# Kernel tuning notes

Hardware: AMD Instinct MI355X
Metric: run time of the kernel (lower is better)

Reference implementation:

```python
import jax, jax.numpy as jnp
import numpy as np

B, T = 256, 1024
IN_DIM, OUT_DIM = 32, 32
STATE_DIM, DIM_NL = 128, 128
EPS = 1e-3            # pos_def_tol
ALPHA = 1.0           # contraction_rate_lb
STD = 0.5             # initialization_std


def setup_inputs() -> dict:
    key = jax.random.key(0)
    ks = jax.random.split(key, 9)
    f = lambda k, sh: jax.random.normal(k, sh, dtype=jnp.float32)
    n, q = STATE_DIM, DIM_NL
    return {
        "x0_sys": f(ks[0], (B, 1, OUT_DIM)),
        "u_in": f(ks[1], (B, T, IN_DIM)),
        "X": f(ks[2], (2 * n + q, 2 * n + q)) * STD,
        "Y": f(ks[3], (n, n)) * STD,
        "B2": f(ks[4], (n, IN_DIM)) * STD,
        "C2": f(ks[5], (OUT_DIM, n)) * STD,
        "D21": f(ks[6], (OUT_DIM, q)) * STD,
        "D22": f(ks[7], (OUT_DIM, IN_DIM)) * STD,
        "D12": f(ks[8], (q, IN_DIM)) * STD,
    }


def _derived(X, Y):
    # Contraction-preserving reparametrization ("_update_model_param").
    n, q = STATE_DIM, DIM_NL
    H = X.T @ X + EPS * jnp.eye(2 * n + q, dtype=X.dtype)
    H11 = H[:n, :n]
    H21 = H[n:n + q, :n]
    H22 = H[n:n + q, n:n + q]
    H31 = H[n + q:, :n]
    H32 = H[n + q:, n:n + q]
    H33 = H[n + q:, n + q:]          # P
    F_ = H31
    B1 = H32
    E = 0.5 * (H11 + ALPHA * H33 + Y - Y.T)
    E_inv = jnp.linalg.inv(E)
    Lam = 0.5 * jnp.diag(H22)
    D11 = -jnp.tril(H22, -1)          # strictly lower triangular
    C1 = -H21
    return F_, B1, E_inv, Lam, D11, C1


def reference(x0_sys, u_in, X, Y, B2, C2, D21, D22, D12):
    F_, B1, E_inv, Lam, D11, C1 = _derived(X, Y)
    q = DIM_NL

    # reset(): x0 = min-norm lstsq solution of C2 x0 = y0_sys  (lstsq == pinv here)
    y0_sys = x0_sys[:, 0, :]                       # (B, out)
    x0 = (jnp.linalg.pinv(C2) @ y0_sys.T).T        # (B, n)
    y0 = x0 @ C2.T                                 # (B, out)

    idx = jnp.arange(q)

    def step(x, u):
        # one REN forward step; x:(B,n), u:(B,in)
        a = x @ C1.T + u @ D12.T                   # (B, q), i-independent part of v

        def inner(w, inp):
            i, d_row, lam, a_i = inp               # a_i:(B,)
            v = a_i + w @ d_row                    # strictly-lower-tri recurrence on w
            return w.at[:, i].set(jnp.tanh(v / lam)), None

        w0 = jnp.zeros((x.shape[0], q), x.dtype)
        w, _ = jax.lax.scan(inner, w0, (idx, D11, Lam, a.T))
        x_new = (x @ F_.T + w @ B1.T + u @ B2.T) @ E_inv.T
        y = x_new @ C2.T + w @ D21.T + u @ D22.T
        return x_new, y

    _, ys = jax.lax.scan(step, x0, jnp.swapaxes(u_in, 0, 1))   # (T, B, out)
    # run() emits y0 then outputs after u[0..T-2] (last step's y is dropped)
    y_traj = jnp.concatenate([y0[None], ys[:-1]], axis=0)      # (T, B, out)
    return jnp.swapaxes(y_traj, 0, 1)                          # (B, T, out)
```

## Files before the change

### kernel.cpp

```cpp
#include <hip/hip_runtime.h>
#include <hip/hip_bf16.h>

#define DEV static __device__ __forceinline__

constexpr int Tn = 1024;
constexpr float LOG2E = 1.4426950408889634f;

constexpr int OFF_H     = 0;
constexpr int OFF_E     = 147456;
constexpr int OFF_EINV  = 163840;
constexpr int OFF_M     = 180224;
constexpr int OFF_MINV  = 181248;
constexpr int OFF_GL2   = 182272;
constexpr int OFF_FH    = 182400;
constexpr int OFF_B1H   = 198784;
constexpr int OFF_B2H   = 215168;
constexpr int OFF_W0    = 219264;
constexpr int OFF_WC    = 223360;
constexpr int OFF_CF    = 227456;
constexpr int OFF_CB    = 243840;
constexpr int OFF_CB2   = 260224;
constexpr int OFF_PF    = 264320;
constexpr int OFF_PB    = 280704;
constexpr int OFF_PCF   = 297088;
constexpr int OFF_PCB   = 313472;
constexpr int OFF_SAB   = 329856;
constexpr int OFF_SB2   = 338048;
constexpr int OFF_BUQ   = 342144;
constexpr int OFF_D12Q  = 346240;
constexpr int OFF_SCB2  = 350336;
constexpr int OFF_WCS   = 354432;
constexpr int OFF_C2Y   = 358528;
constexpr int OFF_D21Y  = 362624;
constexpr int OFF_D22Y  = 366720;
constexpr int OFF_AUG   = 367744;
constexpr int OFF_AUG2  = 400512;
constexpr int OFF_X0    = 402560;
constexpr int OFF_A0    = 435328;
constexpr int WS_FLOATS = 468096;

__device__ __align__(16) float g_ws[WS_FLOATS];
__device__ int g_isf32;
__device__ float4 g_Q [256 * 1024 * 64];
__device__ float2 g_Xs[256 * 1024 * 64];
__device__ float2 g_Ws[256 * 1024 * 64];

DEV float ld(const void* p, int i, int f) {
  return f ? ((const float*)p)[i]
           : __bfloat162float(((const __hip_bfloat16*)p)[i]);
}
DEV float rdlane(float v, int l) {
  return __int_as_float(__builtin_amdgcn_readlane(__float_as_int(v), l));
}

__global__ void k_detect(const void* __restrict__ X) {
  if (threadIdx.x == 0) {
    const __hip_bfloat16* p = (const __hip_bfloat16*)X;
    int bad = 0;
    for (int i = 0; i < 512; ++i) {
      float v = __bfloat162float(p[i]);
      if (!(v > -1e6f && v < 1e6f)) bad++;
    }
    g_isf32 = (bad > 0) ? 1 : 0;
  }
}

__global__ void k_H(const void* __restrict__ X) {
  const int f = g_isf32;
  float* ws = g_ws;
  int id = blockIdx.x * 256 + threadIdx.x;
  int r = id / 384, c = id % 384;
  float acc = 0.f;
  for (int k = 0; k < 384; ++k)
    acc = fmaf(ld(X, k * 384 + r, f), ld(X, k * 384 + c, f), acc);
  if (r == c) acc += 0.001f;
  ws[OFF_H + id] = acc;
}

__global__ void k_derived(const void* __restrict__ Y, const void* __restrict__ C2) {
  const int f = g_isf32;
  float* ws = g_ws;
  const float* H = ws + OFF_H;
  int id = blockIdx.x * 256 + threadIdx.x;
  if (id < 16384) {
    int i = id >> 7, j = id & 127;
    ws[OFF_E + id] = 0.5f * (H[i * 384 + j] + H[(256 + i) * 384 + 256 + j]
                             + ld(Y, i * 128 + j, f) - ld(Y, j * 128 + i, f));
  } else if (id < 16512) {
    int i = id - 16384;
    ws[OFF_GL2 + i] = LOG2E * 4.f / H[(128 + i) * 384 + 128 + i];
  } else if (id < 17536) {
    int t = id - 16512; int a = t >> 5, b = t & 31;
    float acc = 0.f;
    for (int j = 0; j < 128; ++j)
      acc = fmaf(ld(C2, a * 128 + j, f), ld(C2, b * 128 + j, f), acc);
    ws[OFF_M + t] = acc;
  }
}

__global__ void k_inv_lds() {
  extern __shared__ float smv[];
  float* aug  = smv;
  float* aug2 = smv + 32768;
  __shared__ float col[128];
  float* ws = g_ws;
  const float* E = ws + OFF_E;
  int tid = threadIdx.x;
  for (int idx = tid; idx < 32768; idx += 1024) {
    int i = idx >> 8, j = idx & 255;
    aug[idx] = (j < 128) ? E[i * 128 + j] : ((j - 128) == i ? 1.f : 0.f);
  }
  __syncthreads();
  for (int k = 0; k < 128; ++k) {
    if (tid < 128) col[tid] = aug[tid * 256 + k];
    __syncthreads();
    float d = 1.f / col[k];
    if (tid < 256) aug[k * 256 + tid] *= d;
    __syncthreads();
    int j = tid & 255, iseg = tid >> 8;
    float rkj = aug[k * 256 + j];
    for (int i = iseg * 32; i < iseg * 32 + 32; ++i) {
      if (i == k) continue;
      aug[i * 256 + j] -= col[i] * rkj;
    }
    __syncthreads();
  }
  for (int idx = tid; idx < 16384; idx += 1024) {
    int i = idx >> 7, j = idx & 127;
    ws[OFF_EINV + idx] = aug[i * 256 + 128 + j];
  }
  const float* M = ws + OFF_M;
  for (int idx = tid; idx < 2048; idx += 1024) {
    int i = idx >> 6, j = idx & 63;
    aug2[idx] = (j < 32) ? M[i * 32 + j] : ((j - 32) == i ? 1.f : 0.f);
  }
  __syncthreads();
  for (int k = 0; k < 32; ++k) {
    if (tid < 32) col[tid] = aug2[tid * 64 + k];
    __syncthreads();
    float d = 1.f / col[k];
    if (tid < 64) aug2[k * 64 + tid] *= d;
    __syncthreads();
    if (tid < 64) {
      float rkj = aug2[k * 64 + tid];
      for (int i = 0; i < 32; ++i) if (i != k) aug2[i * 64 + tid] -= col[i] * rkj;
    }
    __syncthreads();
  }
  for (int idx = tid; idx < 1024; idx += 1024) {
    int i = idx >> 5, j = idx & 31;
    ws[OFF_MINV + idx] = aug2[i * 64 + 32 + j];
  }
}

__global__ void k_inv() {
  float* ws = g_ws;
  __shared__ float col[128];
  float* aug = ws + OFF_AUG;
  const float* E = ws + OFF_E;
  int tid = threadIdx.x;
  for (int idx = tid; idx < 32768; idx += 1024) {
    int i = idx >> 8, j = idx & 255;
    aug[idx] = (j < 128) ? E[i * 128 + j] : ((j - 128) == i ? 1.f : 0.f);
  }
  __syncthreads();
  for (int k = 0; k < 128; ++k) {
    if (tid < 128) col[tid] = aug[tid * 256 + k];
    __syncthreads();
    float d = 1.f / col[k];
    if (tid < 256) aug[k * 256 + tid] *= d;
    __syncthreads();
    int j = tid & 255, iseg = tid >> 8;
    float rkj = aug[k * 256 + j];
    for (int i = iseg * 32; i < iseg * 32 + 32; ++i) {
      if (i == k) continue;
      aug[i * 256 + j] -= col[i] * rkj;
    }
    __syncthreads();
  }
  for (int idx = tid; idx < 16384; idx += 1024) {
    int i = idx >> 7, j = idx & 127;
    ws[OFF_EINV + idx] = aug[i * 256 + 128 + j];
  }
  __syncthreads();
  float* aug2 = ws + OFF_AUG2;
  const float* M = ws + OFF_M;
  for (int idx = tid; idx < 2048; idx += 1024) {
    int i = idx >> 6, j = idx & 63;
    aug2[idx] = (j < 32) ? M[i * 32 + j] : ((j - 32) == i ? 1.f : 0.f);
  }
  __syncthreads();
  for (int k = 0; k < 32; ++k) {
    if (tid < 32) col[tid] = aug2[tid * 64 + k];
    __syncthreads();
    float d = 1.f / col[k];
    if (tid < 64) aug2[k * 64 + tid] *= d;
    __syncthreads();
    if (tid < 64) {
      float rkj = aug2[k * 64 + tid];
      for (int i = 0; i < 32; ++i) if (i != k) aug2[i * 64 + tid] -= col[i] * rkj;
    }
    __syncthreads();
  }
  for (int idx = tid; idx < 1024; idx += 1024) {
    int i = idx >> 5, j = idx & 31;
    ws[OFF_MINV + idx] = aug2[i * 64 + 32 + j];
  }
}

__global__ void k_fuse(const void* __restrict__ B2, const void* __restrict__ C2) {
  const int f = g_isf32;
  float* ws = g_ws;
  const float* einv = ws + OFF_EINV;
  const float* H = ws + OFF_H;
  const float* minv = ws + OFF_MINV;
  int id = blockIdx.x * 256 + threadIdx.x;
  if (id < 16384) {
    int l = id >> 7, j = id & 127;
    float a = 0.f;
    for (int m = 0; m < 128; ++m) a = fmaf(einv[l * 128 + m], H[(256 + m) * 384 + j], a);
    ws[OFF_FH + id] = a;
  } else if (id < 32768) {
    int t = id - 16384; int l = t >> 7, j = t & 127;
    float a = 0.f;
    for (int m = 0; m < 128; ++m) a = fmaf(einv[l * 128 + m], H[(256 + m) * 384 + 128 + j], a);
    ws[OFF_B1H + t] = a;
  } else if (id < 36864) {
    int t = id - 32768; int l = t >> 5, k = t & 31;
    float a = 0.f;
    for (int m = 0; m < 128; ++m) a = fmaf(einv[l * 128 + m], ld(B2, m * 32 + k, f), a);
    ws[OFF_B2H + t] = a;
  } else if (id < 40960) {
    int t = id - 36864; int k = t >> 7, l = t & 127;
    float a = 0.f;
    for (int m = 0; m < 32; ++m) a = fmaf(minv[k * 32 + m], ld(C2, m * 128 + l, f), a);
    ws[OFF_W0 + t] = a;
  }
}

__global__ void k_w2() {
  float* ws = g_ws;
  const float* H = ws + OFF_H;
  const float* w0 = ws + OFF_W0;
  int id = blockIdx.x * 256 + threadIdx.x;
  int k = id >> 7, l = id & 127;
  float a = 0.f;
  for (int m = 0; m < 128; ++m) a = fmaf(w0[k * 128 + m], -H[(128 + l) * 384 + m], a);
  ws[OFF_WC + id] = a;
}

__global__ void k_cf() {
  float* ws = g_ws;
  const float* H = ws + OFF_H;
  int id = blockIdx.x * 256 + threadIdx.x;
  if (id < 16384) {
    int l = id >> 7, j = id & 127;
    float a = 0.f;
    for (int m = 0; m < 128; ++m) a = fmaf(-H[(128 + l) * 384 + m], ws[OFF_FH + m * 128 + j], a);
    ws[OFF_CF + id] = a;
  } else if (id < 32768) {
    int t = id - 16384; int l = t >> 7, j = t & 127;
    float a = 0.f;
    for (int m = 0; m < 128; ++m) a = fmaf(-H[(128 + l) * 384 + m], ws[OFF_B1H + m * 128 + j], a);
    ws[OFF_CB + t] = a;
  } else {
    int t = id - 32768; int l = t >> 5, k = t & 31;
    float a = 0.f;
    for (int m = 0; m < 128; ++m) a = fmaf(-H[(128 + l) * 384 + m], ws[OFF_B2H + m * 32 + k], a);
    ws[OFF_CB2 + t] = a;
  }
}

__global__ void k_pk(const void* __restrict__ D12, const void* __restrict__ C2,
                     const void* __restrict__ D21, const void* __restrict__ D22) {
  const int f = g_isf32;
  float* ws = g_ws;
  const float* H = ws + OFF_H;
  const float* g = ws + OFF_GL2;
  int id = blockIdx.x * 256 + threadIdx.x;
  if (id < 8192) {
    int j = id >> 6, l = id & 63;
    ((float2*)(ws + OFF_PF))[id] =
        make_float2(ws[OFF_FH + l * 128 + j], ws[OFF_FH + (l + 64) * 128 + j]);
  } else if (id < 16384) {
    int t = id - 8192; int j = t >> 6, l = t & 63;
    ((float2*)(ws + OFF_PB))[t] =
        make_float2(ws[OFF_B1H + l * 128 + j], ws[OFF_B1H + (l + 64) * 128 + j]);
  } else if (id < 24576) {
    int t = id - 16384; int j = t >> 6, l = t & 63;
    ((float2*)(ws + OFF_PCF))[t] =
        make_float2(g[l] * ws[OFF_CF + l * 128 + j], g[l + 64] * ws[OFF_CF + (l + 64) * 128 + j]);
  } else if (id < 32768) {
    int t = id - 24576; int j = t >> 6, l = t & 63;
    ((float2*)(ws + OFF_PCB))[t] =
        make_float2(g[l] * ws[OFF_CB + l * 128 + j], g[l + 64] * ws[OFF_CB + (l + 64) * 128 + j]);
  } else if (id < 36864) {
    int t = id - 32768; int i = t >> 6, l = t & 63;
    float sx = (i < l) ? -g[l] * H[(128 + l) * 384 + 128 + i] : 0.f;
    float sy = -g[l + 64] * H[(192 + l) * 384 + 128 + i];
    ((float2*)(ws + OFF_SAB))[t] = make_float2(sx, sy);
  } else if (id < 40960) {
    int t = id - 36864; int ii = t >> 6, l = t & 63;
    ws[OFF_SB2 + t] = (ii < l) ? -g[l + 64] * H[(192 + l) * 384 + 192 + ii] : 0.f;
  } else if (id < 43008) {
    int t = id - 40960; int k = t >> 6, l = t & 63;
    ((float2*)(ws + OFF_BUQ))[t] =
        make_float2(ws[OFF_B2H + l * 32 + k], ws[OFF_B2H + (l + 64) * 32 + k]);
  } else if (id < 45056) {
    int t = id - 43008; int k = t >> 6, l = t & 63;
    ((float2*)(ws + OFF_D12Q))[t] =
        make_float2(g[l] * ld(D12, l * 32 + k, f), g[l + 64] * ld(D12, (l + 64) * 32 + k, f));
  } else if (id < 47104) {
    int t = id - 45056; int k = t >> 6, l = t & 63;
    ((float2*)(ws + OFF_SCB2))[t] =
        make_float2(g[l] * ws[OFF_CB2 + l * 32 + k], g[l + 64] * ws[OFF_CB2 + (l + 64) * 32 + k]);
  } else if (id < 49152) {
    int t = id - 47104; int k = t >> 6, l = t & 63;
    ((float2*)(ws + OFF_WCS))[t] =
        make_float2(g[l] * ws[OFF_WC + k * 128 + l], g[l + 64] * ws[OFF_WC + k * 128 + l + 64]);
  } else if (id < 53248) {
    int t = id - 49152; int m = t >> 5, o = t & 31;
    ws[OFF_C2Y + t] = ld(C2, o * 128 + m, f);
  } else if (id < 57344) {
    int t = id - 53248; int m = t >> 5, o = t & 31;
    ws[OFF_D21Y + t] = ld(D21, o * 128 + m, f);
  } else if (id < 58368) {
    int t = id - 57344; int k = t >> 5, o = t & 31;
    ws[OFF_D22Y + t] = ld(D22, o * 32 + k, f);
  }
}

__global__ void k_x0a0(const void* __restrict__ x0s, const void* __restrict__ u_in) {
  const int f = g_isf32;
  float* ws = g_ws;
  int id = blockIdx.x * 256 + threadIdx.x;
  if (id < 32768) {
    int b = id >> 7, l = id & 127;
    float a = 0.f;
    for (int k = 0; k < 32; ++k)
      a = fmaf(ld(x0s, b * 32 + k, f), ws[OFF_W0 + k * 128 + l], a);
    ws[OFF_X0 + id] = a;
  } else {
    int t = id - 32768; int b = t >> 6, lane = t & 63;
    const float2* WCs = (const float2*)(ws + OFF_WCS);
    const float2* D12Q = (const float2*)(ws + OFF_D12Q);
    float ax = 0.f, ay = 0.f;
    for (int k = 0; k < 32; ++k) {
      float yk = ld(x0s, b * 32 + k, f);
      float2 wc = WCs[k * 64 + lane];
      ax = fmaf(wc.x, yk, ax); ay = fmaf(wc.y, yk, ay);
      float u0 = ld(u_in, b * Tn * 32 + k, f);
      float2 dq = D12Q[k * 64 + lane];
      ax = fmaf(dq.x, u0, ax); ay = fmaf(dq.y, u0, ay);
    }
    ((float2*)(ws + OFF_A0))[b * 64 + lane] = make_float2(ax, ay);
  }
}

__global__ __launch_bounds__(256) void k_q(const void* __restrict__ u_in) {
  const int f = g_isf32;
  const float* ws = g_ws;
  int lane = threadIdx.x & 63, wave = threadIdx.x >> 6;
  int idx = blockIdx.x * 4 + wave;
  int b = idx >> 10, t = idx & 1023;
  if (t >= Tn - 1) return;
  const float2* BUq = (const float2*)(ws + OFF_BUQ);
  const float2* SCB2 = (const float2*)(ws + OFF_SCB2);
  const float2* D12Q = (const float2*)(ws + OFF_D12Q);
  float bx = 0.f, by = 0.f, ax = 0.f, ay = 0.f;
#pragma unroll 8
  for (int k = 0; k < 32; ++k) {
    float u0 = ld(u_in, (b * Tn + t) * 32 + k, f);
    float2 bu = BUq[k * 64 + lane];
    bx = fmaf(bu.x, u0, bx); by = fmaf(bu.y, u0, by);
    float2 sc = SCB2[k * 64 + lane];
    ax = fmaf(sc.x, u0, ax); ay = fmaf(sc.y, u0, ay);
    float u1 = ld(u_in, (b * Tn + t + 1) * 32 + k, f);
    float2 dq = D12Q[k * 64 + lane];
    ax = fmaf(dq.x, u1, ax); ay = fmaf(dq.y, u1, ay);
  }
  g_Q[((size_t)b * Tn + t) * 64 + lane] = make_float4(bx, by, ax, ay);
}

__global__ __launch_bounds__(512) void k_scan8() {
  __shared__ float2 sSAB[64 * 64];
  __shared__ float  sSB2[64 * 64];
  __shared__ float2 xbuf[2][8][64];
  __shared__ float2 abuf[2][8][64];
  const float* ws = g_ws;
  const int tid = threadIdx.x, lane = tid & 63, w = tid >> 6;
  for (int i = tid; i < 4096; i += 512) sSAB[i] = ((const float2*)(ws + OFF_SAB))[i];
  for (int i = tid; i < 4096; i += 512) sSB2[i] = ws[OFF_SB2 + i];

  const bool isScan = (w < 4);
  float2 vA[32], vB[32];
  {
    const float2* P1 = (const float2*)(ws + (isScan ? OFF_PB : OFF_PF));
    const float2* P2 = (const float2*)(ws + (isScan ? OFF_PCB : OFF_PCF));
    const int jcol = (w & 3) * 32;
#pragma unroll
    for (int c = 0; c < 32; ++c) {
      vA[c] = P1[(jcol + c) * 64 + lane];
      vB[c] = P2[(jcol + c) * 64 + lane];
    }
  }
  const int b = blockIdx.x;
  float xl = ws[OFF_X0 + b * 128 + lane];
  float xh = ws[OFF_X0 + b * 128 + 64 + lane];
  float2 a2 = ((const float2*)(ws + OFF_A0))[b * 64 + lane];
  float accx = a2.x, accy = a2.y;
  const float4* Q = g_Q + (size_t)b * Tn * 64;
  float4 q = make_float4(0.f, 0.f, 0.f, 0.f);
  if (w == 4) q = Q[lane];
  size_t sbase = (size_t)b * Tn * 64 + lane;
  const int jb = __builtin_amdgcn_readfirstlane((w & 1) * 32);
  __syncthreads();

#pragma unroll 1
  for (int t = 0; t < Tn - 1; ++t) {
    const int p = t & 1;
    float px, py, pax, pay;
    if (isScan) {
#pragma unroll
      for (int i = 0; i < 64; ++i) {
        float s = rdlane(accx, i);
        float e2 = __builtin_amdgcn_exp2f(s);
        float wi = fmaf(-2.f, __builtin_amdgcn_rcpf(1.f + e2), 1.f);
        float2 sp = sSAB[i * 64 + lane];
        accx = fmaf(sp.x, wi, accx);
        accy = fmaf(sp.y, wi, accy);
      }
      float ex = __builtin_amdgcn_exp2f(accx);
      float wx = fmaf(-2.f, __builtin_amdgcn_rcpf(1.f + ex), 1.f);
#pragma unroll
      for (int i = 0; i < 64; ++i) {
        float s = rdlane(accy, i);
        float e2 = __builtin_amdgcn_exp2f(s);
        float wi = fmaf(-2.f, __builtin_amdgcn_rcpf(1.f + e2), 1.f);
        accy = fmaf(sSB2[i * 64 + lane], wi, accy);
      }
      float ey = __builtin_amdgcn_exp2f(accy);
      float wy = fmaf(-2.f, __builtin_amdgcn_rcpf(1.f + ey), 1.f);
      if (w == 0) g_Ws[sbase + (size_t)t * 64] = make_float2(wx, wy);

      px = 0.f; py = 0.f; pax = 0.f; pay = 0.f;
      float wsrc = (w < 2) ? wx : wy;
#pragma unroll
      for (int c = 0; c < 32; ++c) {
        float wj = rdlane(wsrc, jb + c);
        px  = fmaf(vA[c].x, wj, px);
        py  = fmaf(vA[c].y, wj, py);
        pax = fmaf(vB[c].x, wj, pax);
        pay = fmaf(vB[c].y, wj, pay);
      }
    } else {
      float4 qn = q;
      if (w == 4 && t + 1 < Tn - 1) qn = Q[(size_t)(t + 1) * 64 + lane];
      if (w == 4) { px = q.x; py = q.y; pax = q.z; pay = q.w; }
      else        { px = 0.f; py = 0.f; pax = 0.f; pay = 0.f; }
      float xsrc = (w < 6) ? xl : xh;
#pragma unroll
      for (int c = 0; c < 32; ++c) {
        float xj = rdlane(xsrc, jb + c);
        px  = fmaf(vA[c].x, xj, px);
        py  = fmaf(vA[c].y, xj, py);
        pax = fmaf(vB[c].x, xj, pax);
        pay = fmaf(vB[c].y, xj, pay);
      }
      q = qn;
    }
    xbuf[p][w][lane] = make_float2(px, py);
    abuf[p][w][lane] = make_float2(pax, pay);
    __syncthreads();

    if (isScan) {
      float sax = 0.f, say = 0.f;
#pragma unroll
      for (int w2 = 0; w2 < 8; ++w2) {
        float2 av = abuf[p][w2][lane];
        sax += av.x; say += av.y;
      }
      accx = sax; accy = say;
    } else {
      float sxl = 0.f, sxh = 0.f;
#pragma unroll
      for (int w2 = 0; w2 < 8; ++w2) {
        float2 xv = xbuf[p][w2][lane];
        sxl += xv.x; sxh += xv.y;
      }
      xl = sxl; xh = sxh;
      if (w == 5) g_Xs[sbase + (size_t)(t + 1) * 64] = make_float2(xl, xh);
    }
  }
}

__global__ __launch_bounds__(256) void k_y(const void* __restrict__ x0s,
                                           const void* __restrict__ u_in,
                                           void* __restrict__ out) {
  const int f = g_isf32;
  const float* ws = g_ws;
  int lane = threadIdx.x & 63, wave = threadIdx.x >> 6;
  int idx = blockIdx.x * 4 + wave;
  int b = idx >> 10, tau = idx & 1023;
  int o = lane & 31, h = lane >> 5;
  if (tau == 0) {
    if (lane < 32) {
      size_t oi = (size_t)b * Tn * 32 + o;
      float v = ld(x0s, b * 32 + o, f);
      if (f) ((float*)out)[oi] = v;
      else   ((__hip_bfloat16*)out)[oi] = __float2bfloat16(v);
    }
    return;
  }
  const float* Xf = (const float*)g_Xs;
  const float* Wf = (const float*)g_Ws;
  const float* C2Y = ws + OFF_C2Y;
  const float* D21Y = ws + OFF_D21Y;
  const float* D22Y = ws + OFF_D22Y;
  size_t rbase = ((size_t)b * Tn + tau) * 128;
  size_t pbase = ((size_t)b * Tn + tau - 1) * 128;
  float acc = 0.f;
#pragma unroll 8
  for (int l = 0; l < 64; ++l)
    acc = fmaf(Xf[rbase + 2 * l + h], C2Y[(l + 64 * h) * 32 + o], acc);
#pragma unroll 8
  for (int l = 0; l < 64; ++l)
    acc = fmaf(Wf[pbase + 2 * l + h], D21Y[(l + 64 * h) * 32 + o], acc);
  if (h == 0) {
#pragma unroll 8
    for (int k = 0; k < 32; ++k)
      acc = fmaf(ld(u_in, (b * Tn + tau - 1) * 32 + k, f), D22Y[k * 32 + o], acc);
  }
  acc += __shfl_down(acc, 32);
  if (lane < 32) {
    size_t oi = ((size_t)b * Tn + tau) * 32 + o;
    if (f) ((float*)out)[oi] = acc;
    else   ((__hip_bfloat16*)out)[oi] = __float2bfloat16(acc);
  }
}

extern "C" void kernel_launch(void* const* d_in, const int* in_sizes, int n_in,
                              void* d_out, int out_size, void* d_ws, size_t ws_size,
                              hipStream_t stream) {
  const void* x0s = d_in[0];
  const void* u   = d_in[1];
  const void* X   = d_in[2];
  const void* Y   = d_in[3];
  const void* B2  = d_in[4];
  const void* C2  = d_in[5];
  const void* D21 = d_in[6];
  const void* D22 = d_in[7];
  const void* D12 = d_in[8];
  (void)d_ws; (void)ws_size; (void)in_sizes; (void)n_in; (void)out_size;

  hipLaunchKernelGGL(k_detect,  dim3(1),     dim3(64),   0, stream, X);
  hipLaunchKernelGGL(k_H,       dim3(576),   dim3(256),  0, stream, X);
  hipLaunchKernelGGL(k_derived, dim3(69),    dim3(256),  0, stream, Y, C2);

  hipError_t e = hipFuncSetAttribute((const void*)k_inv_lds,
                                     hipFuncAttributeMaxDynamicSharedMemorySize,
                                     139264);
  if (e == hipSuccess) {
    hipLaunchKernelGGL(k_inv_lds, dim3(1), dim3(1024), 139264, stream);
  } else {
    (void)hipGetLastError();
    hipLaunchKernelGGL(k_inv,     dim3(1), dim3(1024), 0, stream);
  }

  hipLaunchKernelGGL(k_fuse,    dim3(160),   dim3(256),  0, stream, B2, C2);
  hipLaunchKernelGGL(k_w2,      dim3(16),    dim3(256),  0, stream);
  hipLaunchKernelGGL(k_cf,      dim3(144),   dim3(256),  0, stream);
  hipLaunchKernelGGL(k_pk,      dim3(228),   dim3(256),  0, stream, D12, C2, D21, D22);
  hipLaunchKernelGGL(k_x0a0,    dim3(192),   dim3(256),  0, stream, x0s, u);
  hipLaunchKernelGGL(k_q,       dim3(65536), dim3(256),  0, stream, u);
  hipLaunchKernelGGL(k_scan8,   dim3(256),   dim3(512),  0, stream);
  hipLaunchKernelGGL(k_y,       dim3(65536), dim3(256),  0, stream, x0s, u, d_out);
}
```

Measured before the change: 7.058 ms.

## Fuse input projection and output emission into the sequential scan kernel

Removes the separate k_q and k_y kernels and their large global intermediate buffers (Q, Xs, Ws). The input projections are now computed on the fly by helper waves inside the scan, and the outputs are emitted by a dedicated wave from state held in registers and LDS. Scan waves get raised priority via s_setprio. This cuts a large amount of global memory traffic and two kernel launches. In exchange, the helper waves read weights from global memory every step and the y computation may lengthen the per-step critical path.

```diff
diff --git a/kernel.cpp b/kernel.cpp
--- a/kernel.cpp
+++ b/kernel.cpp
@@ -41,11 +41,8 @@
 
 __device__ __align__(16) float g_ws[WS_FLOATS];
 __device__ int g_isf32;
-__device__ float4 g_Q [256 * 1024 * 64];
-__device__ float2 g_Xs[256 * 1024 * 64];
-__device__ float2 g_Ws[256 * 1024 * 64];
-
-DEV float ld(const void* p, int i, int f) {
+
+DEV float ld(const void* p, size_t i, int f) {
   return f ? ((const float*)p)[i]
            : __bfloat162float(((const __hip_bfloat16*)p)[i]);
 }
@@ -357,46 +354,58 @@
   }
 }
 
-__global__ __launch_bounds__(256) void k_q(const void* __restrict__ u_in) {
-  const int f = g_isf32;
-  const float* ws = g_ws;
-  int lane = threadIdx.x & 63, wave = threadIdx.x >> 6;
-  int idx = blockIdx.x * 4 + wave;
-  int b = idx >> 10, t = idx & 1023;
-  if (t >= Tn - 1) return;
-  const float2* BUq = (const float2*)(ws + OFF_BUQ);
-  const float2* SCB2 = (const float2*)(ws + OFF_SCB2);
-  const float2* D12Q = (const float2*)(ws + OFF_D12Q);
-  float bx = 0.f, by = 0.f, ax = 0.f, ay = 0.f;
+DEV void y_emit(const float* ws, float xlv, float xhv, float2 wv, float uyv,
+                int b, int t, int lane, int f, void* out) {
+  int o = lane & 31, h = lane >> 5;
+  const float* C2Y = ws + OFF_C2Y;
+  const float* D21Y = ws + OFF_D21Y;
+  const float* D22Y = ws + OFF_D22Y;
+  float acc = 0.f;
 #pragma unroll 8
-  for (int k = 0; k < 32; ++k) {
-    float u0 = ld(u_in, (b * Tn + t) * 32 + k, f);
-    float2 bu = BUq[k * 64 + lane];
-    bx = fmaf(bu.x, u0, bx); by = fmaf(bu.y, u0, by);
-    float2 sc = SCB2[k * 64 + lane];
-    ax = fmaf(sc.x, u0, ax); ay = fmaf(sc.y, u0, ay);
-    float u1 = ld(u_in, (b * Tn + t + 1) * 32 + k, f);
-    float2 dq = D12Q[k * 64 + lane];
-    ax = fmaf(dq.x, u1, ax); ay = fmaf(dq.y, u1, ay);
-  }
-  g_Q[((size_t)b * Tn + t) * 64 + lane] = make_float4(bx, by, ax, ay);
-}
-
-__global__ __launch_bounds__(512) void k_scan8() {
+  for (int l = 0; l < 64; ++l) {
+    float xle = rdlane(xlv, l), xhe = rdlane(xhv, l);
+    float xv = h ? xhe : xle;
+    acc = fmaf(xv, C2Y[(l + 64 * h) * 32 + o], acc);
+  }
+#pragma unroll 8
+  for (int l = 0; l < 64; ++l) {
+    float wxe = rdlane(wv.x, l), wye = rdlane(wv.y, l);
+    float wvv = h ? wye : wxe;
+    acc = fmaf(wvv, D21Y[(l + 64 * h) * 32 + o], acc);
+  }
+  if (h == 0) {
+#pragma unroll 8
+    for (int k = 0; k < 32; ++k)
+      acc = fmaf(rdlane(uyv, k), D22Y[k * 32 + o], acc);
+  }
+  acc += __shfl_down(acc, 32);
+  if (lane < 32) {
+    size_t oi = ((size_t)b * Tn + t) * 32 + o;
+    if (f) ((float*)out)[oi] = acc;
+    else   ((__hip_bfloat16*)out)[oi] = __float2bfloat16(acc);
+  }
+}
+
+__global__ __launch_bounds__(512) void k_scan8(const void* __restrict__ u_in,
+                                               const void* __restrict__ x0s,
+                                               void* __restrict__ out) {
   __shared__ float2 sSAB[64 * 64];
   __shared__ float  sSB2[64 * 64];
   __shared__ float2 xbuf[2][8][64];
   __shared__ float2 abuf[2][8][64];
   const float* ws = g_ws;
+  const int f = g_isf32;
   const int tid = threadIdx.x, lane = tid & 63, w = tid >> 6;
   for (int i = tid; i < 4096; i += 512) sSAB[i] = ((const float2*)(ws + OFF_SAB))[i];
   for (int i = tid; i < 4096; i += 512) sSB2[i] = ws[OFF_SB2 + i];
 
+  const int b = blockIdx.x;
   const bool isScan = (w < 4);
+
   float2 vA[32], vB[32];
-  {
-    const float2* P1 = (const float2*)(ws + (isScan ? OFF_PB : OFF_PF));
-    const float2* P2 = (const float2*)(ws + (isScan ? OFF_PCB : OFF_PCF));
+  if (isScan) {
+    const float2* P1 = (const float2*)(ws + OFF_PB);
+    const float2* P2 = (const float2*)(ws + OFF_PCB);
     const int jcol = (w & 3) * 32;
 #pragma unroll
     for (int c = 0; c < 32; ++c) {
@@ -404,23 +413,34 @@
       vB[c] = P2[(jcol + c) * 64 + lane];
     }
   }
-  const int b = blockIdx.x;
   float xl = ws[OFF_X0 + b * 128 + lane];
   float xh = ws[OFF_X0 + b * 128 + 64 + lane];
   float2 a2 = ((const float2*)(ws + OFF_A0))[b * 64 + lane];
   float accx = a2.x, accy = a2.y;
-  const float4* Q = g_Q + (size_t)b * Tn * 64;
-  float4 q = make_float4(0.f, 0.f, 0.f, 0.f);
-  if (w == 4) q = Q[lane];
-  size_t sbase = (size_t)b * Tn * 64 + lane;
+
+  float ucur = 0.f;
+  float u0v = 0.f, u1v = 0.f;
+  float uyc = 0.f;
+  if (w == 4 && lane < 32) ucur = ld(u_in, (size_t)b * Tn * 32 + lane, f);
+  if (w == 6 && lane < 32) {
+    u0v = ld(u_in, (size_t)b * Tn * 32 + lane, f);
+    u1v = ld(u_in, ((size_t)b * Tn + 1) * 32 + lane, f);
+  }
+  if (w == 6) { xbuf[0][6][lane] = make_float2(0.f, 0.f); xbuf[1][6][lane] = make_float2(0.f, 0.f); }
+  if (w == 7 && lane < 32) {
+    size_t oi = (size_t)b * Tn * 32 + lane;
+    float v = ld(x0s, b * 32 + lane, f);
+    if (f) ((float*)out)[oi] = v;
+    else   ((__hip_bfloat16*)out)[oi] = __float2bfloat16(v);
+  }
   const int jb = __builtin_amdgcn_readfirstlane((w & 1) * 32);
   __syncthreads();
 
 #pragma unroll 1
   for (int t = 0; t < Tn - 1; ++t) {
     const int p = t & 1;
-    float px, py, pax, pay;
     if (isScan) {
+      __builtin_amdgcn_s_setprio(1);
 #pragma unroll
       for (int i = 0; i < 64; ++i) {
         float s = rdlane(accx, i);
@@ -441,9 +461,9 @@
       }
       float ey = __builtin_amdgcn_exp2f(accy);
       float wy = fmaf(-2.f, __builtin_amdgcn_rcpf(1.f + ey), 1.f);
-      if (w == 0) g_Ws[sbase + (size_t)t * 64] = make_float2(wx, wy);
-
-      px = 0.f; py = 0.f; pax = 0.f; pay = 0.f;
+      if (w == 0) xbuf[p][7][lane] = make_float2(wx, wy);
+
+      float px = 0.f, py = 0.f, pax = 0.f, pay = 0.f;
       float wsrc = (w < 2) ? wx : wy;
 #pragma unroll
       for (int c = 0; c < 32; ++c) {
@@ -453,89 +473,118 @@
         pax = fmaf(vB[c].x, wj, pax);
         pay = fmaf(vB[c].y, wj, pay);
       }
-    } else {
-      float4 qn = q;
-      if (w == 4 && t + 1 < Tn - 1) qn = Q[(size_t)(t + 1) * 64 + lane];
-      if (w == 4) { px = q.x; py = q.y; pax = q.z; pay = q.w; }
-      else        { px = 0.f; py = 0.f; pax = 0.f; pay = 0.f; }
-      float xsrc = (w < 6) ? xl : xh;
-#pragma unroll
-      for (int c = 0; c < 32; ++c) {
-        float xj = rdlane(xsrc, jb + c);
-        px  = fmaf(vA[c].x, xj, px);
-        py  = fmaf(vA[c].y, xj, py);
-        pax = fmaf(vB[c].x, xj, pax);
-        pay = fmaf(vB[c].y, xj, pay);
-      }
-      q = qn;
-    }
-    xbuf[p][w][lane] = make_float2(px, py);
-    abuf[p][w][lane] = make_float2(pax, pay);
-    __syncthreads();
-
-    if (isScan) {
+      __builtin_amdgcn_s_setprio(0);
+      if (w != 0) xbuf[p][w][lane] = make_float2(px, py);
+      else        xbuf[p][0][lane] = make_float2(px, py);
+      abuf[p][w][lane] = make_float2(pax, pay);
+      __syncthreads();
       float sax = 0.f, say = 0.f;
 #pragma unroll
-      for (int w2 = 0; w2 < 8; ++w2) {
+      for (int w2 = 0; w2 < 7; ++w2) {
         float2 av = abuf[p][w2][lane];
         sax += av.x; say += av.y;
       }
       accx = sax; accy = say;
-    } else {
+    } else if (w == 4) {
+      float un = ucur;
+      if (lane < 32) un = ld(u_in, ((size_t)b * Tn + t + 1) * 32 + lane, f);
+      float px = 0.f, py = 0.f, pax = 0.f, pay = 0.f;
+      const float2* BUq = (const float2*)(ws + OFF_BUQ);
+#pragma unroll 8
+      for (int k = 0; k < 32; ++k) {
+        float uk = rdlane(ucur, k);
+        float2 bu = BUq[k * 64 + lane];
+        px = fmaf(bu.x, uk, px); py = fmaf(bu.y, uk, py);
+      }
+      const float2* PF = (const float2*)(ws + OFF_PF);
+      const float2* PCF = (const float2*)(ws + OFF_PCF);
+#pragma unroll 8
+      for (int c = 0; c < 64; ++c) {
+        float xj = rdlane(xl, c);
+        float2 fv = PF[c * 64 + lane];
+        float2 cv = PCF[c * 64 + lane];
+        px  = fmaf(fv.x, xj, px);  py  = fmaf(fv.y, xj, py);
+        pax = fmaf(cv.x, xj, pax); pay = fmaf(cv.y, xj, pay);
+      }
+      ucur = un;
+      xbuf[p][4][lane] = make_float2(px, py);
+      abuf[p][4][lane] = make_float2(pax, pay);
+      __syncthreads();
       float sxl = 0.f, sxh = 0.f;
 #pragma unroll
-      for (int w2 = 0; w2 < 8; ++w2) {
+      for (int w2 = 0; w2 < 7; ++w2) {
         float2 xv = xbuf[p][w2][lane];
         sxl += xv.x; sxh += xv.y;
       }
       xl = sxl; xh = sxh;
-      if (w == 5) g_Xs[sbase + (size_t)(t + 1) * 64] = make_float2(xl, xh);
-    }
-  }
-}
-
-__global__ __launch_bounds__(256) void k_y(const void* __restrict__ x0s,
-                                           const void* __restrict__ u_in,
-                                           void* __restrict__ out) {
-  const int f = g_isf32;
-  const float* ws = g_ws;
-  int lane = threadIdx.x & 63, wave = threadIdx.x >> 6;
-  int idx = blockIdx.x * 4 + wave;
-  int b = idx >> 10, tau = idx & 1023;
-  int o = lane & 31, h = lane >> 5;
-  if (tau == 0) {
-    if (lane < 32) {
-      size_t oi = (size_t)b * Tn * 32 + o;
-      float v = ld(x0s, b * 32 + o, f);
-      if (f) ((float*)out)[oi] = v;
-      else   ((__hip_bfloat16*)out)[oi] = __float2bfloat16(v);
-    }
-    return;
-  }
-  const float* Xf = (const float*)g_Xs;
-  const float* Wf = (const float*)g_Ws;
-  const float* C2Y = ws + OFF_C2Y;
-  const float* D21Y = ws + OFF_D21Y;
-  const float* D22Y = ws + OFF_D22Y;
-  size_t rbase = ((size_t)b * Tn + tau) * 128;
-  size_t pbase = ((size_t)b * Tn + tau - 1) * 128;
-  float acc = 0.f;
+    } else if (w == 5) {
+      float px = 0.f, py = 0.f, pax = 0.f, pay = 0.f;
+      const float2* PF = (const float2*)(ws + OFF_PF);
+      const float2* PCF = (const float2*)(ws + OFF_PCF);
 #pragma unroll 8
-  for (int l = 0; l < 64; ++l)
-    acc = fmaf(Xf[rbase + 2 * l + h], C2Y[(l + 64 * h) * 32 + o], acc);
+      for (int c = 0; c < 64; ++c) {
+        float xj = rdlane(xh, c);
+        float2 fv = PF[(64 + c) * 64 + lane];
+        float2 cv = PCF[(64 + c) * 64 + lane];
+        px  = fmaf(fv.x, xj, px);  py  = fmaf(fv.y, xj, py);
+        pax = fmaf(cv.x, xj, pax); pay = fmaf(cv.y, xj, pay);
+      }
+      xbuf[p][5][lane] = make_float2(px, py);
+      abuf[p][5][lane] = make_float2(pax, pay);
+      __syncthreads();
+      float sxl = 0.f, sxh = 0.f;
+#pragma unroll
+      for (int w2 = 0; w2 < 7; ++w2) {
+        float2 xv = xbuf[p][w2][lane];
+        sxl += xv.x; sxh += xv.y;
+      }
+      xl = sxl; xh = sxh;
+    } else if (w == 6) {
+      float u2v = u1v;
+      if (lane < 32 && t + 2 < Tn) u2v = ld(u_in, ((size_t)b * Tn + t + 2) * 32 + lane, f);
+      float pax = 0.f, pay = 0.f;
+      const float2* SC = (const float2*)(ws + OFF_SCB2);
+      const float2* DQ = (const float2*)(ws + OFF_D12Q);
 #pragma unroll 8
-  for (int l = 0; l < 64; ++l)
-    acc = fmaf(Wf[pbase + 2 * l + h], D21Y[(l + 64 * h) * 32 + o], acc);
-  if (h == 0) {
-#pragma unroll 8
-    for (int k = 0; k < 32; ++k)
-      acc = fmaf(ld(u_in, (b * Tn + tau - 1) * 32 + k, f), D22Y[k * 32 + o], acc);
-  }
-  acc += __shfl_down(acc, 32);
-  if (lane < 32) {
-    size_t oi = ((size_t)b * Tn + tau) * 32 + o;
-    if (f) ((float*)out)[oi] = acc;
-    else   ((__hip_bfloat16*)out)[oi] = __float2bfloat16(acc);
+      for (int k = 0; k < 32; ++k) {
+        float u0k = rdlane(u0v, k);
+        float2 sc = SC[k * 64 + lane];
+        pax = fmaf(sc.x, u0k, pax); pay = fmaf(sc.y, u0k, pay);
+        float u1k = rdlane(u1v, k);
+        float2 dq = DQ[k * 64 + lane];
+        pax = fmaf(dq.x, u1k, pax); pay = fmaf(dq.y, u1k, pay);
+      }
+      u0v = u1v; u1v = u2v;
+      abuf[p][6][lane] = make_float2(pax, pay);
+      __syncthreads();
+      float sxl = 0.f, sxh = 0.f;
+#pragma unroll
+      for (int w2 = 0; w2 < 7; ++w2) {
+        float2 xv = xbuf[p][w2][lane];
+        sxl += xv.x; sxh += xv.y;
+      }
+      xl = sxl; xh = sxh;
+    } else {
+      float uyn = uyc;
+      if (lane < 32) uyn = ld(u_in, ((size_t)b * Tn + t) * 32 + lane, f);
+      if (t >= 1) {
+        float2 wv = xbuf[(t - 1) & 1][7][lane];
+        y_emit(ws, xl, xh, wv, uyc, b, t, lane, f, out);
+      }
+      uyc = uyn;
+      __syncthreads();
+      float sxl = 0.f, sxh = 0.f;
+#pragma unroll
+      for (int w2 = 0; w2 < 7; ++w2) {
+        float2 xv = xbuf[p][w2][lane];
+        sxl += xv.x; sxh += xv.y;
+      }
+      xl = sxl; xh = sxh;
+    }
+  }
+  if (w == 7) {
+    float2 wv = xbuf[(Tn - 2) & 1][7][lane];
+    y_emit(ws, xl, xh, wv, uyc, b, Tn - 1, lane, f, out);
   }
 }
 
@@ -572,7 +621,5 @@
   hipLaunchKernelGGL(k_cf,      dim3(144),   dim3(256),  0, stream);
   hipLaunchKernelGGL(k_pk,      dim3(228),   dim3(256),  0, stream, D12, C2, D21, D22);
   hipLaunchKernelGGL(k_x0a0,    dim3(192),   dim3(256),  0, stream, x0s, u);
-  hipLaunchKernelGGL(k_q,       dim3(65536), dim3(256),  0, stream, u);
-  hipLaunchKernelGGL(k_scan8,   dim3(256),   dim3(512),  0, stream);
-  hipLaunchKernelGGL(k_y,       dim3(65536), dim3(256),  0, stream, x0s, u, d_out);
-}
+  hipLaunchKernelGGL(k_scan8,   dim3(256),   dim3(512),  0, stream, u, x0s, d_out);
+}
```

Result: faster. 6.603 ms (-6.5%).

## Stage weights in LDS and batch timesteps per block in precompute and output kernels

Applied to the files above, without the earlier changes.

Rewrites k_q and k_y as persistent-per-batch kernels with 512 threads. Each block stages its weight matrices into shared memory once and loops over timesteps, where the old kernels launched 65536 small blocks that each reread the weights from global memory. Input rows are loaded coalesced once per wave and broadcast to lanes with readlane, replacing per-lane scalar loads. The scan kernel also moves its barrier and reduction into each branch, which is a structural tidy-up. The trade-off is only 256 blocks, which may underfill the GPU and lowers parallelism for these memory-bound kernels.

```diff
diff --git a/kernel.cpp b/kernel.cpp
--- a/kernel.cpp
+++ b/kernel.cpp
@@ -45,7 +45,7 @@
 __device__ float2 g_Xs[256 * 1024 * 64];
 __device__ float2 g_Ws[256 * 1024 * 64];
 
-DEV float ld(const void* p, int i, int f) {
+DEV float ld(const void* p, size_t i, int f) {
   return f ? ((const float*)p)[i]
            : __bfloat162float(((const __hip_bfloat16*)p)[i]);
 }
@@ -357,29 +357,38 @@
   }
 }
 
-__global__ __launch_bounds__(256) void k_q(const void* __restrict__ u_in) {
-  const int f = g_isf32;
+__global__ __launch_bounds__(512) void k_q2(const void* __restrict__ u_in) {
+  __shared__ float2 sBUQ[2048], sSCB2[2048], sD12Q[2048];
   const float* ws = g_ws;
-  int lane = threadIdx.x & 63, wave = threadIdx.x >> 6;
-  int idx = blockIdx.x * 4 + wave;
-  int b = idx >> 10, t = idx & 1023;
-  if (t >= Tn - 1) return;
-  const float2* BUq = (const float2*)(ws + OFF_BUQ);
-  const float2* SCB2 = (const float2*)(ws + OFF_SCB2);
-  const float2* D12Q = (const float2*)(ws + OFF_D12Q);
-  float bx = 0.f, by = 0.f, ax = 0.f, ay = 0.f;
+  const int f = g_isf32;
+  const int tid = threadIdx.x, lane = tid & 63, w = tid >> 6;
+  for (int i = tid; i < 2048; i += 512) {
+    sBUQ[i]  = ((const float2*)(ws + OFF_BUQ))[i];
+    sSCB2[i] = ((const float2*)(ws + OFF_SCB2))[i];
+    sD12Q[i] = ((const float2*)(ws + OFF_D12Q))[i];
+  }
+  __syncthreads();
+  const int b = blockIdx.x;
+  for (int t = w; t < Tn - 1; t += 8) {
+    float uc = 0.f, un = 0.f;
+    if (lane < 32) {
+      uc = ld(u_in, ((size_t)b * Tn + t) * 32 + lane, f);
+      un = ld(u_in, ((size_t)b * Tn + t + 1) * 32 + lane, f);
+    }
+    float bx = 0.f, by = 0.f, ax = 0.f, ay = 0.f;
 #pragma unroll 8
-  for (int k = 0; k < 32; ++k) {
-    float u0 = ld(u_in, (b * Tn + t) * 32 + k, f);
-    float2 bu = BUq[k * 64 + lane];
-    bx = fmaf(bu.x, u0, bx); by = fmaf(bu.y, u0, by);
-    float2 sc = SCB2[k * 64 + lane];
-    ax = fmaf(sc.x, u0, ax); ay = fmaf(sc.y, u0, ay);
-    float u1 = ld(u_in, (b * Tn + t + 1) * 32 + k, f);
-    float2 dq = D12Q[k * 64 + lane];
-    ax = fmaf(dq.x, u1, ax); ay = fmaf(dq.y, u1, ay);
-  }
-  g_Q[((size_t)b * Tn + t) * 64 + lane] = make_float4(bx, by, ax, ay);
+    for (int k = 0; k < 32; ++k) {
+      float u0 = rdlane(uc, k);
+      float2 bu = sBUQ[k * 64 + lane];
+      bx = fmaf(bu.x, u0, bx); by = fmaf(bu.y, u0, by);
+      float2 sc = sSCB2[k * 64 + lane];
+      ax = fmaf(sc.x, u0, ax); ay = fmaf(sc.y, u0, ay);
+      float u1 = rdlane(un, k);
+      float2 dq = sD12Q[k * 64 + lane];
+      ax = fmaf(dq.x, u1, ax); ay = fmaf(dq.y, u1, ay);
+    }
+    g_Q[((size_t)b * Tn + t) * 64 + lane] = make_float4(bx, by, ax, ay);
+  }
 }
 
 __global__ __launch_bounds__(512) void k_scan8() {
@@ -419,7 +428,6 @@
 #pragma unroll 1
   for (int t = 0; t < Tn - 1; ++t) {
     const int p = t & 1;
-    float px, py, pax, pay;
     if (isScan) {
 #pragma unroll
       for (int i = 0; i < 64; ++i) {
@@ -443,7 +451,7 @@
       float wy = fmaf(-2.f, __builtin_amdgcn_rcpf(1.f + ey), 1.f);
       if (w == 0) g_Ws[sbase + (size_t)t * 64] = make_float2(wx, wy);
 
-      px = 0.f; py = 0.f; pax = 0.f; pay = 0.f;
+      float px = 0.f, py = 0.f, pax = 0.f, pay = 0.f;
       float wsrc = (w < 2) ? wx : wy;
 #pragma unroll
       for (int c = 0; c < 32; ++c) {
@@ -453,9 +461,20 @@
         pax = fmaf(vB[c].x, wj, pax);
         pay = fmaf(vB[c].y, wj, pay);
       }
+      xbuf[p][w][lane] = make_float2(px, py);
+      abuf[p][w][lane] = make_float2(pax, pay);
+      __syncthreads();
+      float sax = 0.f, say = 0.f;
+#pragma unroll
+      for (int w2 = 0; w2 < 8; ++w2) {
+        float2 av = abuf[p][w2][lane];
+        sax += av.x; say += av.y;
+      }
+      accx = sax; accy = say;
     } else {
       float4 qn = q;
       if (w == 4 && t + 1 < Tn - 1) qn = Q[(size_t)(t + 1) * 64 + lane];
+      float px, py, pax, pay;
       if (w == 4) { px = q.x; py = q.y; pax = q.z; pay = q.w; }
       else        { px = 0.f; py = 0.f; pax = 0.f; pay = 0.f; }
       float xsrc = (w < 6) ? xl : xh;
@@ -468,20 +487,9 @@
         pay = fmaf(vB[c].y, xj, pay);
       }
       q = qn;
-    }
-    xbuf[p][w][lane] = make_float2(px, py);
-    abuf[p][w][lane] = make_float2(pax, pay);
-    __syncthreads();
-
-    if (isScan) {
-      float sax = 0.f, say = 0.f;
-#pragma unroll
-      for (int w2 = 0; w2 < 8; ++w2) {
-        float2 av = abuf[p][w2][lane];
-        sax += av.x; say += av.y;
-      }
-      accx = sax; accy = say;
-    } else {
+      xbuf[p][w][lane] = make_float2(px, py);
+      abuf[p][w][lane] = make_float2(pax, pay);
+      __syncthreads();
       float sxl = 0.f, sxh = 0.f;
 #pragma unroll
       for (int w2 = 0; w2 < 8; ++w2) {
@@ -494,48 +502,56 @@
   }
 }
 
-__global__ __launch_bounds__(256) void k_y(const void* __restrict__ x0s,
-                                           const void* __restrict__ u_in,
-                                           void* __restrict__ out) {
-  const int f = g_isf32;
+__global__ __launch_bounds__(512) void k_y2(const void* __restrict__ x0s,
+                                            const void* __restrict__ u_in,
+                                            void* __restrict__ out) {
+  __shared__ float sC2Y[4096], sD21Y[4096], sD22Y[1024];
   const float* ws = g_ws;
-  int lane = threadIdx.x & 63, wave = threadIdx.x >> 6;
-  int idx = blockIdx.x * 4 + wave;
-  int b = idx >> 10, tau = idx & 1023;
-  int o = lane & 31, h = lane >> 5;
-  if (tau == 0) {
+  const int f = g_isf32;
+  const int tid = threadIdx.x, lane = tid & 63, w = tid >> 6;
+  for (int i = tid; i < 4096; i += 512) { sC2Y[i] = ws[OFF_C2Y + i]; sD21Y[i] = ws[OFF_D21Y + i]; }
+  for (int i = tid; i < 1024; i += 512) sD22Y[i] = ws[OFF_D22Y + i];
+  __syncthreads();
+  const int b = blockIdx.x;
+  const int o = lane & 31, h = lane >> 5;
+  for (int t = w; t < Tn; t += 8) {
+    if (t == 0) {
+      if (lane < 32) {
+        size_t oi = (size_t)b * Tn * 32 + o;
+        float v = ld(x0s, b * 32 + o, f);
+        if (f) ((float*)out)[oi] = v;
+        else   ((__hip_bfloat16*)out)[oi] = __float2bfloat16(v);
+      }
+      continue;
+    }
+    float2 xv2 = g_Xs[((size_t)b * Tn + t) * 64 + lane];
+    float2 wv  = g_Ws[((size_t)b * Tn + t - 1) * 64 + lane];
+    float uy = 0.f;
+    if (lane < 32) uy = ld(u_in, ((size_t)b * Tn + t - 1) * 32 + lane, f);
+    float acc = 0.f;
+#pragma unroll 8
+    for (int l = 0; l < 64; ++l) {
+      float xle = rdlane(xv2.x, l), xhe = rdlane(xv2.y, l);
+      float xvv = h ? xhe : xle;
+      acc = fmaf(xvv, sC2Y[(l + 64 * h) * 32 + o], acc);
+    }
+#pragma unroll 8
+    for (int l = 0; l < 64; ++l) {
+      float wxe = rdlane(wv.x, l), wye = rdlane(wv.y, l);
+      float wvv = h ? wye : wxe;
+      acc = fmaf(wvv, sD21Y[(l + 64 * h) * 32 + o], acc);
+    }
+    if (h == 0) {
+#pragma unroll 8
+      for (int k = 0; k < 32; ++k)
+        acc = fmaf(rdlane(uy, k), sD22Y[k * 32 + o], acc);
+    }
+    acc += __shfl_down(acc, 32);
     if (lane < 32) {
-      size_t oi = (size_t)b * Tn * 32 + o;
-      float v = ld(x0s, b * 32 + o, f);
-      if (f) ((float*)out)[oi] = v;
-      else   ((__hip_bfloat16*)out)[oi] = __float2bfloat16(v);
-    }
-    return;
-  }
-  const float* Xf = (const float*)g_Xs;
-  const float* Wf = (const float*)g_Ws;
-  const float* C2Y = ws + OFF_C2Y;
-  const float* D21Y = ws + OFF_D21Y;
-  const float* D22Y = ws + OFF_D22Y;
-  size_t rbase = ((size_t)b * Tn + tau) * 128;
-  size_t pbase = ((size_t)b * Tn + tau - 1) * 128;
-  float acc = 0.f;
-#pragma unroll 8
-  for (int l = 0; l < 64; ++l)
-    acc = fmaf(Xf[rbase + 2 * l + h], C2Y[(l + 64 * h) * 32 + o], acc);
-#pragma unroll 8
-  for (int l = 0; l < 64; ++l)
-    acc = fmaf(Wf[pbase + 2 * l + h], D21Y[(l + 64 * h) * 32 + o], acc);
-  if (h == 0) {
-#pragma unroll 8
-    for (int k = 0; k < 32; ++k)
-      acc = fmaf(ld(u_in, (b * Tn + tau - 1) * 32 + k, f), D22Y[k * 32 + o], acc);
-  }
-  acc += __shfl_down(acc, 32);
-  if (lane < 32) {
-    size_t oi = ((size_t)b * Tn + tau) * 32 + o;
-    if (f) ((float*)out)[oi] = acc;
-    else   ((__hip_bfloat16*)out)[oi] = __float2bfloat16(acc);
+      size_t oi = ((size_t)b * Tn + t) * 32 + o;
+      if (f) ((float*)out)[oi] = acc;
+      else   ((__hip_bfloat16*)out)[oi] = __float2bfloat16(acc);
+    }
   }
 }
 
@@ -572,7 +588,7 @@
   hipLaunchKernelGGL(k_cf,      dim3(144),   dim3(256),  0, stream);
   hipLaunchKernelGGL(k_pk,      dim3(228),   dim3(256),  0, stream, D12, C2, D21, D22);
   hipLaunchKernelGGL(k_x0a0,    dim3(192),   dim3(256),  0, stream, x0s, u);
-  hipLaunchKernelGGL(k_q,       dim3(65536), dim3(256),  0, stream, u);
+  hipLaunchKernelGGL(k_q2,      dim3(256),   dim3(512),  0, stream, u);
   hipLaunchKernelGGL(k_scan8,   dim3(256),   dim3(512),  0, stream);
-  hipLaunchKernelGGL(k_y,       dim3(65536), dim3(256),  0, stream, x0s, u, d_out);
-}
+  hipLaunchKernelGGL(k_y2,      dim3(256),   dim3(512),  0, stream, x0s, u, d_out);
+}
```

Result: faster. 6.043 ms (median of 2 runs) (-14.4%).
